# Kernel tuning notes

Measured on AMD Instinct MI355X. Metric: run time of the kernel, lower is better.

The kernel has to match this reference:

```python
import jax, jax.numpy as jnp
import numpy as np

B, T, A, K, STEPS, E = 2, 16384, 128, 128, 16, 126


def soft_dirac_last(x):
    # softmax forward-replaced by one-hot(argmax), straight-through backward
    sm = jax.nn.softmax(x, axis=-1)
    hard = jax.nn.one_hot(jnp.argmax(x, axis=-1), x.shape[-1], dtype=x.dtype)
    return sm + jax.lax.stop_gradient(hard - sm)


def _encode(x, d_unit, atom_embeddings):
    # x: (B,1,T); d_unit: (A,K) unit-norm atoms
    rng = jnp.linspace(0.0, 1.0, T, dtype=x.dtype)
    kernel = d_unit[:, None, :]  # OIH
    pad = [(K // 2, K - 1 - K // 2)]  # SAME
    batch_ix = jnp.arange(B)

    def step(res, _):
        # dense feature map: correlation of residual with every atom
        fm = jax.lax.conv_general_dilated(
            res, kernel, window_strides=(1,), padding=pad,
            dimension_numbers=("NCH", "OIH", "NCH"))  # (B,A,T)
        flat = fm.reshape(B, A * T)
        fi = jnp.argmax(flat, axis=-1)                      # sparsify n_to_keep=1
        value = jnp.take_along_axis(flat, fi[:, None], axis=-1)  # (B,1)
        ai = fi // T
        ti = fi % T
        # position: soft_dirac over time of sparse fm summed over atoms
        pos_row = jnp.zeros((B, T), x.dtype).at[batch_ix, ti].set(value[:, 0])
        pd = soft_dirac_last(pos_row)
        position = jnp.sum(pd * rng[None, :], axis=-1, keepdims=True) * 20.0  # (B,1)
        # atom one-hot: soft_dirac over atom axis of sparse fm summed over time
        atom_row = jnp.zeros((B, A), x.dtype).at[batch_ix, ai].set(value[:, 0])
        ad = soft_dirac_last(atom_row)
        ae = ad @ atom_embeddings  # (B,E)
        emb = jnp.concatenate([position, value, ae], axis=-1)  # (B, 2+E)
        # matching-pursuit residual update: subtract value * atom at found shift
        recon = value * d_unit[ai]  # (B,K)
        buf = jnp.zeros((B, T + K), x.dtype)
        buf = jax.vmap(lambda bb, rr, tt: jax.lax.dynamic_update_slice(bb, rr, (tt,)))(buf, recon, ti)
        res = res - buf[:, None, K // 2:K // 2 + T]
        return res, emb

    res, embs = jax.lax.scan(step, x, None, length=STEPS)
    embs = jnp.transpose(embs, (1, 0, 2))  # (B, STEPS, 2+E)
    return embs, res


def _canonical_ordering(embs, proj):
    keys = embs @ proj  # (B, STEPS)
    order = jnp.argsort(keys, axis=-1)
    return jnp.take_along_axis(embs, order[:, :, None], axis=1)


def setup_inputs() -> dict:
    key = jax.random.key(0)
    ks = jax.random.split(key, 5)
    return {
        "a": jax.random.normal(ks[0], (B, 1, T), jnp.float32),
        "b": jax.random.normal(ks[1], (B, 1, T), jnp.float32),
        "d": jax.random.normal(ks[2], (A, K), jnp.float32),
        "atom_embeddings": jax.random.normal(ks[3], (A, E), jnp.float32) * 0.1,
        "ordering_proj": jax.random.normal(ks[4], (128,), jnp.float32),
    }


def reference(a, b, d, atom_embeddings, ordering_proj):
    d_unit = d / (jnp.linalg.norm(d, axis=-1, keepdims=True) + 1e-8)
    ae, a_res = _encode(a, d_unit, atom_embeddings)
    be, b_res = _encode(b, d_unit, atom_embeddings)
    ae = _canonical_ordering(ae, ordering_proj)
    be = _canonical_ordering(be, ordering_proj)
    a_norm = jnp.linalg.norm(a_res.reshape(-1, T), axis=-1)
    b_norm = jnp.linalg.norm(b_res.reshape(-1, T), axis=-1)
    return jnp.mean((ae - be) ** 2) + jnp.mean(jnp.abs(a_norm - b_norm))
```

## Files before the change

kernel.cpp:

```cpp
#include <hip/hip_runtime.h>
#include <math.h>

#define T_DIM 16384
#define A_DIM 128
#define K_DIM 128
#define N_STEPS 16
#define E_DIM 126
#define NSEQ 4

#define ATI 16
#define TT 256
#define NTT 64
#define NPT 512
#define INC_B 16
#define RS_PAD 392

__device__ inline unsigned long long pack_vi(float v, int fi) {
    unsigned int b = __float_as_uint(v);
    b = (b & 0x80000000u) ? ~b : (b | 0x80000000u);
    return ((unsigned long long)b << 32) | (unsigned int)(~fi);
}
__device__ inline void unpack_vi(unsigned long long p, float* v, int* fi) {
    unsigned int lo = (unsigned int)(p & 0xffffffffu);
    unsigned int b = (unsigned int)(p >> 32);
    unsigned int fb = (b & 0x80000000u) ? (b & 0x7fffffffu) : ~b;
    *v = __uint_as_float(fb);
    *fi = (int)(~lo);
}

__global__ __launch_bounds__(256) void k_prep(
    const float* __restrict__ d, const float* __restrict__ a,
    const float* __restrict__ b, float* __restrict__ du,
    float* __restrict__ res, int* __restrict__ cnt,
    unsigned long long* __restrict__ slots) {
    int blk = blockIdx.x, tid = threadIdx.x;
    if (blk < 128) {
        __shared__ float s[128];
        float v = 0.0f;
        if (tid < 128) { v = d[blk * K_DIM + tid]; s[tid] = v * v; }
        __syncthreads();
        for (int off = 64; off > 0; off >>= 1) {
            if (tid < off) s[tid] += s[tid + off];
            __syncthreads();
        }
        if (tid < 128) du[blk * K_DIM + tid] = v / (sqrtf(s[0]) + 1e-8f);
    } else if (blk < 384) {
        int i = (blk - 128) * 256 + tid;
        res[i] = (i < 2 * T_DIM) ? a[i] : b[i - 2 * T_DIM];
    } else {
        if (tid < NSEQ) cnt[tid] = 0;
        for (int i = tid; i < (N_STEPS - 1) * NSEQ * INC_B; i += 256) slots[i] = 0ULL;
    }
}

__device__ inline unsigned long long tile_fast(
    const float* __restrict__ res, const float* __restrict__ du,
    int seq, int a_base, int t0, int tid,
    float* res_sh, unsigned long long* red4,
    const float* val_h, const int* ti_h, const int* ai_h, int nh) {

    const float* resS = res + seq * T_DIM;
    for (int i = tid; i < RS_PAD; i += 256) {
        int t = t0 + i - K_DIM / 2;
        float v = 0.0f;
        if (t >= 0 && t < T_DIM && i < TT + K_DIM - 1) {
            v = resS[t];
            for (int s = 0; s < nh; s++) {
                int dk = t - (ti_h[s] - K_DIM / 2);
                if (dk >= 0 && dk < K_DIM)
                    v = __fsub_rn(v, __fmul_rn(val_h[s], du[ai_h[s] * K_DIM + dk]));
            }
        }
        res_sh[i] = v;
    }
    __syncthreads();

    int tg = tid & 63;
    int ag = __builtin_amdgcn_readfirstlane(tid >> 6);
    const float* duP = du + (a_base + ag * 4) * K_DIM;

    float acc[4][4];
    #pragma unroll
    for (int i = 0; i < 4; i++)
        #pragma unroll
        for (int j = 0; j < 4; j++) acc[i][j] = 0.0f;

    float r[8];
    *(float2*)&r[0] = *(const float2*)&res_sh[4 * tg + 0];
    *(float2*)&r[2] = *(const float2*)&res_sh[4 * tg + 2];
    *(float2*)&r[4] = *(const float2*)&res_sh[4 * tg + 4];
    *(float2*)&r[6] = *(const float2*)&res_sh[4 * tg + 6];

    #pragma unroll 4
    for (int k = 0; k < K_DIM; k += 4) {
        float dA[4][4];
        #pragma unroll
        for (int i = 0; i < 4; i++)
            *(float4*)dA[i] = *(const float4*)(duP + i * K_DIM + k);
        #pragma unroll
        for (int dk = 0; dk < 4; dk++) {
            #pragma unroll
            for (int i = 0; i < 4; i++) {
                float s = dA[i][dk];
                #pragma unroll
                for (int j = 0; j < 4; j++)
                    acc[i][j] = fmaf(s, r[j + dk], acc[i][j]);
            }
        }
        r[0] = r[4]; r[1] = r[5]; r[2] = r[6]; r[3] = r[7];
        *(float2*)&r[4] = *(const float2*)&res_sh[4 * tg + k + 8];
        *(float2*)&r[6] = *(const float2*)&res_sh[4 * tg + k + 10];
    }

    float bv = -INFINITY;
    int bi = 0x7fffffff;
    #pragma unroll
    for (int i = 0; i < 4; i++) {
        int a = a_base + ag * 4 + i;
        #pragma unroll
        for (int j = 0; j < 4; j++) {
            int t = t0 + 4 * tg + j;
            int fi = a * T_DIM + t;
            float v = acc[i][j];
            if (v > bv || (v == bv && fi < bi)) { bv = v; bi = fi; }
        }
    }
    #pragma unroll
    for (int off = 32; off > 0; off >>= 1) {
        float v2 = __shfl_down(bv, off);
        int   i2 = __shfl_down(bi, off);
        if (v2 > bv || (v2 == bv && i2 < bi)) { bv = v2; bi = i2; }
    }
    if ((tid & 63) == 0) red4[tid >> 6] = pack_vi(bv, bi);
    __syncthreads();
    if (tid == 0) {
        unsigned long long m = red4[0];
        #pragma unroll
        for (int w = 1; w < 4; w++) if (red4[w] > m) m = red4[w];
        red4[0] = m;
    }
    __syncthreads();
    return red4[0];
}

__global__ __launch_bounds__(256) void k_step_full(
    float* __restrict__ res, const float* __restrict__ du,
    const float* __restrict__ ae, float* __restrict__ emb,
    unsigned long long* __restrict__ pmax, int* __restrict__ cnt,
    int* __restrict__ dirty0) {

    int seq = blockIdx.y;
    int blk = blockIdx.x;
    int a_base = (blk >> 6) * ATI;
    int t0 = (blk & 63) * TT;
    int tid = threadIdx.x;

    alignas(16) __shared__ float res_sh[RS_PAD];
    __shared__ unsigned long long red4[4];
    __shared__ unsigned long long pm_sh[256];
    __shared__ int last_flag;

    unsigned long long p = tile_fast(res, du, seq, a_base, t0, tid,
                                     res_sh, red4, nullptr, nullptr, nullptr, 0);
    if (tid == 0) {
        pmax[seq * NPT + blk] = p;
        __threadfence();
        last_flag = (atomicAdd(&cnt[seq], 1) == NPT - 1);
    }
    __syncthreads();
    if (!last_flag) return;

    __threadfence();
    {
        unsigned long long m0 = pmax[seq * NPT + tid];
        unsigned long long m1 = pmax[seq * NPT + 256 + tid];
        pm_sh[tid] = m0 > m1 ? m0 : m1;
    }
    __syncthreads();
    for (int off = 128; off > 0; off >>= 1) {
        if (tid < off) { if (pm_sh[tid + off] > pm_sh[tid]) pm_sh[tid] = pm_sh[tid + off]; }
        __syncthreads();
    }
    float value; int fi;
    unpack_vi(pm_sh[0], &value, &fi);
    int ai = fi >> 14;
    int ti = fi & (T_DIM - 1);
    int pos_idx = value > 0.0f ? ti : 0;
    int atom_idx = value > 0.0f ? ai : 0;

    float* e = emb + (seq * N_STEPS + 0) * 128;
    if (tid == 0) {
        e[0] = ((float)pos_idx / (float)(T_DIM - 1)) * 20.0f;
        e[1] = value;
        int nlo = ti - (K_DIM - 1); if (nlo < 0) nlo = 0;
        int nhi = ti + K_DIM;       if (nhi > T_DIM) nhi = T_DIM;
        dirty0[seq * 2 + 0] = nlo;
        dirty0[seq * 2 + 1] = nhi;
    }
    if (tid >= 2 && tid < 2 + E_DIM) e[tid] = ae[atom_idx * E_DIM + tid - 2];
    if (tid >= 128) {
        int k = tid - 128;
        int t = ti + k - K_DIM / 2;
        if (t >= 0 && t < T_DIM) {
            float r = res[seq * T_DIM + t];
            res[seq * T_DIM + t] = __fsub_rn(r, __fmul_rn(value, du[ai * K_DIM + k]));
        }
    }
}

__global__ __launch_bounds__(256) void k_inc(
    float* __restrict__ res, const float* __restrict__ du,
    const float* __restrict__ ae, float* __restrict__ emb,
    const unsigned long long* __restrict__ pmax,
    unsigned long long* __restrict__ slots, const int* __restrict__ dirty0) {

    int seq = blockIdx.y;
    int blk = blockIdx.x;
    int atile = blk >> 1;
    int par = blk & 1;
    int a_base = atile * ATI;
    int tid = threadIdx.x;

    alignas(16) __shared__ float res_sh[RS_PAD];
    __shared__ unsigned long long red4[4];
    __shared__ unsigned long long tmax[32];
    __shared__ unsigned long long poll_sh[INC_B];
    __shared__ float val_h[N_STEPS - 1];
    __shared__ int   ti_h[N_STEPS - 1];
    __shared__ int   ai_h[N_STEPS - 1];
    __shared__ int   lo_sh, hi_sh;

    if (tid < 32) tmax[tid] = pmax[seq * NPT + atile * NTT + par + 2 * tid];
    int lo = dirty0[seq * 2 + 0];
    int hi = dirty0[seq * 2 + 1];
    __syncthreads();

    for (int step = 1; step < N_STEPS; step++) {
        int T0 = lo >> 8;
        int tt = ((T0 & 1) == par) ? T0 : T0 + 1;
        bool valid = (tt < NTT) && (tt * TT < hi);

        if (valid) {
            unsigned long long p = tile_fast(res, du, seq, a_base, tt * TT,
                                             tid, res_sh, red4,
                                             val_h, ti_h, ai_h, step - 1);
            if (tid == 0) tmax[(tt - par) >> 1] = p;
        }
        if (tid == 0) {
            unsigned long long m = tmax[0];
            for (int j = 1; j < 32; j++) if (tmax[j] > m) m = tmax[j];
            atomicExch(&slots[((step - 1) * NSEQ + seq) * INC_B + blk], m);
        }
        if (tid < INC_B) {
            const unsigned long long* sp =
                &slots[((step - 1) * NSEQ + seq) * INC_B + tid];
            unsigned long long v = __hip_atomic_load(sp, __ATOMIC_RELAXED,
                                                     __HIP_MEMORY_SCOPE_AGENT);
            while (v == 0ULL) {
                __builtin_amdgcn_s_sleep(1);
                v = __hip_atomic_load(sp, __ATOMIC_RELAXED,
                                      __HIP_MEMORY_SCOPE_AGENT);
            }
            poll_sh[tid] = v;
        }
        __syncthreads();
        if (tid == 0) {
            unsigned long long w = poll_sh[0];
            for (int j = 1; j < INC_B; j++) if (poll_sh[j] > w) w = poll_sh[j];
            float value; int fi;
            unpack_vi(w, &value, &fi);
            int ti = fi & (T_DIM - 1);
            val_h[step - 1] = value;
            ti_h[step - 1] = ti;
            ai_h[step - 1] = fi >> 14;
            int nlo = ti - (K_DIM - 1); if (nlo < 0) nlo = 0;
            int nhi = ti + K_DIM;       if (nhi > T_DIM) nhi = T_DIM;
            lo_sh = nlo; hi_sh = nhi;
        }
        __syncthreads();

        if (blk == 0) {
            float value = val_h[step - 1];
            int ti = ti_h[step - 1], ai = ai_h[step - 1];
            int pos_idx = value > 0.0f ? ti : 0;
            int atom_idx = value > 0.0f ? ai : 0;
            float* e = emb + (seq * N_STEPS + step) * 128;
            if (tid == 0) {
                e[0] = ((float)pos_idx / (float)(T_DIM - 1)) * 20.0f;
                e[1] = value;
            }
            if (tid >= 2 && tid < 128) e[tid] = ae[atom_idx * E_DIM + tid - 2];
        }
        lo = lo_sh; hi = hi_sh;
    }

    if (blk == 0) {
        __syncthreads();
        for (int s = 0; s < N_STEPS - 1; s++) {
            if (tid < 128) {
                int t = ti_h[s] - K_DIM / 2 + tid;
                if (t >= 0 && t < T_DIM) {
                    float r = res[seq * T_DIM + t];
                    res[seq * T_DIM + t] =
                        __fsub_rn(r, __fmul_rn(val_h[s], du[ai_h[s] * K_DIM + tid]));
                }
            }
            __syncthreads();
        }
    }
}

__global__ __launch_bounds__(1024) void k_tail(
    const float* __restrict__ res, const float* __restrict__ emb,
    const float* __restrict__ proj, float* __restrict__ out) {
    int tid = threadIdx.x;
    __shared__ float sh[1024];
    __shared__ float norms[NSEQ];
    __shared__ float keys[NSEQ][N_STEPS];
    __shared__ int   order[NSEQ][N_STEPS];

    {
        int seq = tid >> 8;
        int ln  = tid & 255;
        const float4* r4 = (const float4*)(res + seq * T_DIM);
        float s = 0.0f;
        #pragma unroll
        for (int j = 0; j < 16; j++) {
            float4 v = r4[j * 256 + ln];
            s = fmaf(v.x, v.x, s); s = fmaf(v.y, v.y, s);
            s = fmaf(v.z, v.z, s); s = fmaf(v.w, v.w, s);
        }
        sh[tid] = s;
        __syncthreads();
        for (int off = 128; off > 0; off >>= 1) {
            if (ln < off) sh[tid] += sh[tid + off];
            __syncthreads();
        }
        if (ln == 0) norms[seq] = sqrtf(sh[tid]);
        __syncthreads();
    }
    {
        int pair = tid >> 4;
        int seq = pair >> 4, st = pair & 15;
        int ln = tid & 15;
        const float* e = emb + (seq * N_STEPS + st) * 128 + ln * 8;
        const float* pr = proj + ln * 8;
        float kk = 0.0f;
        #pragma unroll
        for (int dd = 0; dd < 8; dd++) kk = fmaf(e[dd], pr[dd], kk);
        sh[tid] = kk;
        __syncthreads();
        for (int off = 8; off > 0; off >>= 1) {
            if (ln < off) sh[tid] += sh[tid + off];
            __syncthreads();
        }
        if (ln == 0) keys[seq][st] = sh[tid];
        __syncthreads();
    }
    if (tid < NSEQ) {
        int ord[N_STEPS];
        for (int i = 0; i < N_STEPS; i++) ord[i] = i;
        for (int i = 1; i < N_STEPS; i++) {
            int oi = ord[i];
            float kv = keys[tid][oi];
            int j = i - 1;
            while (j >= 0 && keys[tid][ord[j]] > kv) { ord[j + 1] = ord[j]; j--; }
            ord[j + 1] = oi;
        }
        for (int i = 0; i < N_STEPS; i++) order[tid][i] = ord[i];
    }
    __syncthreads();
    float s = 0.0f;
    #pragma unroll
    for (int t = 0; t < 4; t++) {
        int idx = tid + t * 1024;
        int b  = idx >> 11;
        int st = (idx >> 7) & 15;
        int dd = idx & 127;
        float va = emb[((b    ) * N_STEPS + order[b    ][st]) * 128 + dd];
        float vb = emb[((2 + b) * N_STEPS + order[2 + b][st]) * 128 + dd];
        float df = va - vb;
        s = fmaf(df, df, s);
    }
    sh[tid] = s;
    __syncthreads();
    for (int off = 512; off > 0; off >>= 1) {
        if (tid < off) sh[tid] += sh[tid + off];
        __syncthreads();
    }
    if (tid == 0) {
        float mse = sh[0] / 4096.0f;
        float mad = 0.5f * (fabsf(norms[0] - norms[2]) + fabsf(norms[1] - norms[3]));
        out[0] = mse + mad;
    }
}

extern "C" void kernel_launch(void* const* d_in, const int* in_sizes, int n_in,
                              void* d_out, int out_size, void* d_ws, size_t ws_size,
                              hipStream_t stream) {
    const float* a    = (const float*)d_in[0];
    const float* b    = (const float*)d_in[1];
    const float* d    = (const float*)d_in[2];
    const float* ae   = (const float*)d_in[3];
    const float* proj = (const float*)d_in[4];
    float* out = (float*)d_out;

    float* ws  = (float*)d_ws;
    float* res = ws;
    float* du  = res + NSEQ * T_DIM;
    float* emb = du + A_DIM * K_DIM;
    unsigned long long* pmax  = (unsigned long long*)(emb + NSEQ * N_STEPS * 128);
    unsigned long long* slots = pmax + NSEQ * NPT;
    int* cnt    = (int*)(slots + (N_STEPS - 1) * NSEQ * INC_B);
    int* dirty0 = cnt + NSEQ;

    k_prep<<<385, 256, 0, stream>>>(d, a, b, du, res, cnt, slots);

    dim3 gfull(NPT, NSEQ);
    k_step_full<<<gfull, 256, 0, stream>>>(res, du, ae, emb, pmax, cnt, dirty0);

    dim3 ginc(INC_B, NSEQ);
    k_inc<<<ginc, 256, 0, stream>>>(res, du, ae, emb, pmax, slots, dirty0);

    k_tail<<<1, 1024, 0, stream>>>(res, emb, proj, out);
}
```

Before: 252.1 us.

## Keep half-sequence residual resident in LDS across incremental matching-pursuit steps

The incremental kernel now splits each sequence into two halves and gives every block a persistent LDS copy of its half-residual plus halo. Each step's atom subtraction is applied directly in shared memory, so blocks no longer re-read the residual from global memory and replay the whole subtraction history for every tile. Block count per sequence doubles to 32, which adds more slots to poll at each grid-wide step barrier. LDS use grows to roughly 34 KB per block, and a padded indexing scheme is added to avoid bank conflicts.

```diff
diff --git a/kernel.cpp b/kernel.cpp
--- a/kernel.cpp
+++ b/kernel.cpp
@@ -10,10 +10,15 @@
 
 #define ATI 16
 #define TT 256
-#define NTT 64
 #define NPT 512
-#define INC_B 16
-#define RS_PAD 392
+#define INC_B 32
+#define HB 8192
+#define RL_LEN 8319
+#define RL_PAD 8608
+#define SS_LEN 383
+#define SS_PAD 404
+
+#define PIDX(i) ((i) + ((i) >> 5))
 
 __device__ inline unsigned long long pack_vi(float v, int fi) {
     unsigned int b = __float_as_uint(v);
@@ -53,31 +58,9 @@
     }
 }
 
-__device__ inline unsigned long long tile_fast(
-    const float* __restrict__ res, const float* __restrict__ du,
-    int seq, int a_base, int t0, int tid,
-    float* res_sh, unsigned long long* red4,
-    const float* val_h, const int* ti_h, const int* ai_h, int nh) {
-
-    const float* resS = res + seq * T_DIM;
-    for (int i = tid; i < RS_PAD; i += 256) {
-        int t = t0 + i - K_DIM / 2;
-        float v = 0.0f;
-        if (t >= 0 && t < T_DIM && i < TT + K_DIM - 1) {
-            v = resS[t];
-            for (int s = 0; s < nh; s++) {
-                int dk = t - (ti_h[s] - K_DIM / 2);
-                if (dk >= 0 && dk < K_DIM)
-                    v = __fsub_rn(v, __fmul_rn(val_h[s], du[ai_h[s] * K_DIM + dk]));
-            }
-        }
-        res_sh[i] = v;
-    }
-    __syncthreads();
-
-    int tg = tid & 63;
-    int ag = __builtin_amdgcn_readfirstlane(tid >> 6);
-    const float* duP = du + (a_base + ag * 4) * K_DIM;
+__device__ inline unsigned long long tile_compute(
+    const float* __restrict__ duP, const float* __restrict__ rsh,
+    int L0, int a_lo, int t_lo, int tid, unsigned long long* red4) {
 
     float acc[4][4];
     #pragma unroll
@@ -86,10 +69,8 @@
         for (int j = 0; j < 4; j++) acc[i][j] = 0.0f;
 
     float r[8];
-    *(float2*)&r[0] = *(const float2*)&res_sh[4 * tg + 0];
-    *(float2*)&r[2] = *(const float2*)&res_sh[4 * tg + 2];
-    *(float2*)&r[4] = *(const float2*)&res_sh[4 * tg + 4];
-    *(float2*)&r[6] = *(const float2*)&res_sh[4 * tg + 6];
+    #pragma unroll
+    for (int m = 0; m < 8; m++) r[m] = rsh[PIDX(L0 + m)];
 
     #pragma unroll 4
     for (int k = 0; k < K_DIM; k += 4) {
@@ -108,18 +89,18 @@
             }
         }
         r[0] = r[4]; r[1] = r[5]; r[2] = r[6]; r[3] = r[7];
-        *(float2*)&r[4] = *(const float2*)&res_sh[4 * tg + k + 8];
-        *(float2*)&r[6] = *(const float2*)&res_sh[4 * tg + k + 10];
+        #pragma unroll
+        for (int m = 0; m < 4; m++) r[4 + m] = rsh[PIDX(L0 + k + 8 + m)];
     }
 
     float bv = -INFINITY;
     int bi = 0x7fffffff;
     #pragma unroll
     for (int i = 0; i < 4; i++) {
-        int a = a_base + ag * 4 + i;
+        int a = a_lo + i;
         #pragma unroll
         for (int j = 0; j < 4; j++) {
-            int t = t0 + 4 * tg + j;
+            int t = t_lo + j;
             int fi = a * T_DIM + t;
             float v = acc[i][j];
             if (v > bv || (v == bv && fi < bi)) { bv = v; bi = fi; }
@@ -155,13 +136,23 @@
     int t0 = (blk & 63) * TT;
     int tid = threadIdx.x;
 
-    alignas(16) __shared__ float res_sh[RS_PAD];
+    __shared__ float rsh[SS_PAD];
     __shared__ unsigned long long red4[4];
     __shared__ unsigned long long pm_sh[256];
     __shared__ int last_flag;
 
-    unsigned long long p = tile_fast(res, du, seq, a_base, t0, tid,
-                                     res_sh, red4, nullptr, nullptr, nullptr, 0);
+    const float* resS = res + seq * T_DIM;
+    for (int i = tid; i < SS_LEN; i += 256) {
+        int t = t0 - 64 + i;
+        rsh[PIDX(i)] = (t >= 0 && t < T_DIM) ? resS[t] : 0.0f;
+    }
+    __syncthreads();
+
+    int tg = tid & 63;
+    int ag = __builtin_amdgcn_readfirstlane(tid >> 6);
+    unsigned long long p = tile_compute(du + (a_base + ag * 4) * K_DIM, rsh,
+                                        4 * tg, a_base + ag * 4, t0 + 4 * tg,
+                                        tid, red4);
     if (tid == 0) {
         pmax[seq * NPT + blk] = p;
         __threadfence();
@@ -216,39 +207,62 @@
 
     int seq = blockIdx.y;
     int blk = blockIdx.x;
-    int atile = blk >> 1;
+    int atile = blk >> 2;
+    int half = (blk >> 1) & 1;
     int par = blk & 1;
     int a_base = atile * ATI;
+    int base = half * HB;
     int tid = threadIdx.x;
 
-    alignas(16) __shared__ float res_sh[RS_PAD];
+    __shared__ float resL[RL_PAD];
     __shared__ unsigned long long red4[4];
-    __shared__ unsigned long long tmax[32];
+    __shared__ unsigned long long tmax[16];
     __shared__ unsigned long long poll_sh[INC_B];
-    __shared__ float val_h[N_STEPS - 1];
-    __shared__ int   ti_h[N_STEPS - 1];
-    __shared__ int   ai_h[N_STEPS - 1];
-    __shared__ int   lo_sh, hi_sh;
-
-    if (tid < 32) tmax[tid] = pmax[seq * NPT + atile * NTT + par + 2 * tid];
+    __shared__ float val_s;
+    __shared__ int   ti_s, ai_s, lo_sh, hi_sh;
+
+    const float* resG = res + seq * T_DIM;
+    for (int i4 = tid * 4; i4 < RL_LEN; i4 += 1024) {
+        int t = base - 64 + i4;
+        if (t >= 0 && t + 3 < T_DIM && i4 + 3 < RL_LEN) {
+            float4 v = *(const float4*)&resG[t];
+            resL[PIDX(i4 + 0)] = v.x; resL[PIDX(i4 + 1)] = v.y;
+            resL[PIDX(i4 + 2)] = v.z; resL[PIDX(i4 + 3)] = v.w;
+        } else {
+            for (int m = 0; m < 4 && i4 + m < RL_LEN; m++) {
+                int t2 = t + m;
+                resL[PIDX(i4 + m)] = (t2 >= 0 && t2 < T_DIM) ? resG[t2] : 0.0f;
+            }
+        }
+    }
+    if (tid < 16) {
+        int tt = half * 32 + par + 2 * tid;
+        tmax[tid] = pmax[seq * NPT + atile * 64 + tt];
+    }
     int lo = dirty0[seq * 2 + 0];
     int hi = dirty0[seq * 2 + 1];
     __syncthreads();
 
     for (int step = 1; step < N_STEPS; step++) {
         int T0 = lo >> 8;
-        int tt = ((T0 & 1) == par) ? T0 : T0 + 1;
-        bool valid = (tt < NTT) && (tt * TT < hi);
-
-        if (valid) {
-            unsigned long long p = tile_fast(res, du, seq, a_base, tt * TT,
-                                             tid, res_sh, red4,
-                                             val_h, ti_h, ai_h, step - 1);
-            if (tid == 0) tmax[(tt - par) >> 1] = p;
+        int cand = -1;
+        if (((T0 & 1) == par) && ((T0 >> 5) == half)) cand = T0;
+        int T1 = T0 + 1;
+        if (T1 < 64 && ((T1 & 1) == par) && ((T1 >> 5) == half) && T1 * TT < hi)
+            cand = T1;
+
+        if (cand >= 0) {
+            int t0 = cand * TT;
+            int tg = tid & 63;
+            int ag = __builtin_amdgcn_readfirstlane(tid >> 6);
+            unsigned long long p = tile_compute(
+                du + (a_base + ag * 4) * K_DIM, resL,
+                (t0 - base) + 4 * tg, a_base + ag * 4, t0 + 4 * tg, tid, red4);
+            if (tid == 0) tmax[(cand - half * 32 - par) >> 1] = p;
         }
         if (tid == 0) {
             unsigned long long m = tmax[0];
-            for (int j = 1; j < 32; j++) if (tmax[j] > m) m = tmax[j];
+            for (int j = 1; j < 16; j++) if (tmax[j] > m) m = tmax[j];
             atomicExch(&slots[((step - 1) * NSEQ + seq) * INC_B + blk], m);
         }
         if (tid < INC_B) {
@@ -270,9 +284,7 @@
             float value; int fi;
             unpack_vi(w, &value, &fi);
             int ti = fi & (T_DIM - 1);
-            val_h[step - 1] = value;
-            ti_h[step - 1] = ti;
-            ai_h[step - 1] = fi >> 14;
+            val_s = value; ti_s = ti; ai_s = fi >> 14;
             int nlo = ti - (K_DIM - 1); if (nlo < 0) nlo = 0;
             int nhi = ti + K_DIM;       if (nhi > T_DIM) nhi = T_DIM;
             lo_sh = nlo; hi_sh = nhi;
@@ -280,8 +292,8 @@
         __syncthreads();
 
         if (blk == 0) {
-            float value = val_h[step - 1];
-            int ti = ti_h[step - 1], ai = ai_h[step - 1];
+            float value = val_s;
+            int ti = ti_s, ai = ai_s;
             int pos_idx = value > 0.0f ? ti : 0;
             int atom_idx = value > 0.0f ? ai : 0;
             float* e = emb + (seq * N_STEPS + step) * 128;
@@ -291,22 +303,23 @@
             }
             if (tid >= 2 && tid < 128) e[tid] = ae[atom_idx * E_DIM + tid - 2];
         }
-        lo = lo_sh; hi = hi_sh;
-    }
-
-    if (blk == 0) {
-        __syncthreads();
-        for (int s = 0; s < N_STEPS - 1; s++) {
-            if (tid < 128) {
-                int t = ti_h[s] - K_DIM / 2 + tid;
-                if (t >= 0 && t < T_DIM) {
-                    float r = res[seq * T_DIM + t];
-                    res[seq * T_DIM + t] =
-                        __fsub_rn(r, __fmul_rn(val_h[s], du[ai_h[s] * K_DIM + tid]));
+        if (tid < 128) {
+            int t = ti_s - K_DIM / 2 + tid;
+            if (t >= 0 && t < T_DIM) {
+                int L = t - base + 64;
+                if (L >= 0 && L < RL_LEN) {
+                    float r = resL[PIDX(L)];
+                    resL[PIDX(L)] = __fsub_rn(r, __fmul_rn(val_s, du[ai_s * K_DIM + tid]));
                 }
             }
-            __syncthreads();
-        }
+        }
+        __syncthreads();
+        lo = lo_sh; hi = hi_sh;
+    }
+
+    if (atile == 0 && par == 0) {
+        float* resW = res + seq * T_DIM + base;
+        for (int t = tid; t < HB; t += 256) resW[t] = resL[PIDX(t + 64)];
     }
 }
 
```

New measurement: 243.8 us. 3.3% less time.
